# Optimization experiments

Measured on AMD Instinct MI355X. Metric: run time of the kernel, lower is better.

Reference implementation:

```python
import jax, jax.numpy as jnp
import numpy as np

MEX_C = 2.0 / (np.sqrt(3.0) * np.pi ** 0.25)

def mexican_hat(z):
    return MEX_C * (z * z - 1.0) * jnp.exp(-0.5 * z * z)

def setup_inputs() -> dict:
    key = jax.random.key(0)
    ks = jax.random.split(key, 5)
    B, T, D, O = 4, 2048, 128, 128
    x = jax.random.normal(ks[0], (B, T, D), dtype=jnp.float32)
    # init like torch: scale ~ U(0.5,1.5), translation ~ U(-0.5,0.5), kaiming-ish weights
    scale = jax.random.uniform(ks[1], (O, D), dtype=jnp.float32, minval=0.5, maxval=1.5)
    translation = jax.random.uniform(ks[2], (O, D), dtype=jnp.float32, minval=-0.5, maxval=0.5)
    bound = 1.0 / np.sqrt(D)
    wavelet_weights = jax.random.uniform(ks[3], (O, D), dtype=jnp.float32, minval=-bound, maxval=bound)
    base_w = jax.random.uniform(ks[4], (O, D), dtype=jnp.float32, minval=-bound, maxval=bound)
    ln_gamma = jnp.ones((D,), dtype=jnp.float32)
    ln_beta = jnp.zeros((D,), dtype=jnp.float32)
    return {"x": x, "scale": scale, "translation": translation,
            "wavelet_weights": wavelet_weights, "base_w": base_w,
            "ln_gamma": ln_gamma, "ln_beta": ln_beta}

def reference(x, scale, translation, wavelet_weights, base_w, ln_gamma, ln_beta):
    B, T, D = x.shape
    O = wavelet_weights.shape[0]
    # LayerNorm over last dim (eps = 1e-5, torch default)
    mu = jnp.mean(x, axis=-1, keepdims=True)
    var = jnp.mean((x - mu) ** 2, axis=-1, keepdims=True)
    x_norm = (x - mu) / jnp.sqrt(var + 1e-5) * ln_gamma + ln_beta
    x_flat = x_norm.reshape(B * T, D)                      # (N, D)
    s = jax.nn.softplus(scale) + 0.1                       # (O, D)
    # broadcast intermediate (N, O, D) — the memory-bound path
    z = (x_flat[:, None, :] - translation[None]) / s[None]
    w = jnp.clip(mexican_hat(z), -10.0, 10.0)              # (N, O, D)
    wavelet_out = jnp.einsum('nod,od->no', w, wavelet_weights)
    base_out = x.reshape(B * T, D) @ base_w.T              # base uses raw x
    out = wavelet_out + jax.nn.silu(base_out)
    return out.reshape(B, T, O)
```

## Files before the change

kernel.cpp:

```cpp
#include <hip/hip_runtime.h>


#define D_DIM 128
#define O_DIM 128
#define ROWS  16
#define BLOCK 1024
#define XSTRIDE 9

#define C1     0.72134752f
#define SQRT_C 0.84932180f
#define WWK    1.2023651f
#define LOG2E  1.44269504f

typedef float v2f __attribute__((ext_vector_type(2)));

__device__ __forceinline__ unsigned bf16r(float f) {
    unsigned u = __float_as_uint(f);
    return (u + 0x7fffu + ((u >> 16) & 1u)) >> 16;
}


__device__ __forceinline__ v2f pk_fma_xhi_nlo(v2f x, v2f w) {
    v2f d;
    asm("v_pk_fma_f32 %0, %1, %2, %2 op_sel:[0,1,0] op_sel_hi:[1,1,0] neg_lo:[0,0,1] neg_hi:[0,0,1]"
        : "=v"(d) : "v"(x), "v"(w));
    return d;
}
__device__ __forceinline__ v2f pk_mul(v2f a, v2f b) {
    v2f d;
    asm("v_pk_mul_f32 %0, %1, %2" : "=v"(d) : "v"(a), "v"(b));
    return d;
}
__device__ __forceinline__ v2f pk_sub(v2f a, v2f b) {
    v2f d;
    asm("v_pk_add_f32 %0, %1, %2 neg_lo:[0,1] neg_hi:[0,1]" : "=v"(d) : "v"(a), "v"(b));
    return d;
}
__device__ __forceinline__ void pk_fma_acc_lo(v2f& acc, v2f s, v2f w) {
    asm("v_pk_fma_f32 %0, %1, %2, %0 op_sel:[0,0,0] op_sel_hi:[1,0,1]"
        : "+v"(acc) : "v"(s), "v"(w));
}
__device__ __forceinline__ void pk_fma_acc_hi(v2f& acc, v2f s, v2f w) {
    asm("v_pk_fma_f32 %0, %1, %2, %0 op_sel:[0,1,0] op_sel_hi:[1,1,1]"
        : "+v"(acc) : "v"(s), "v"(w));
}

__global__ __launch_bounds__(256) void wavekan_prep(
    const float* __restrict__ scale,
    const float* __restrict__ trans,
    const float* __restrict__ ww,
    const float* __restrict__ bw,
    uint2* __restrict__ wsW)
{
    int idx = blockIdx.x * blockDim.x + threadIdx.x;
    if (idx >= O_DIM * D_DIM) return;
    int o = idx >> 7;
    int d = idx & (D_DIM - 1);
    float sc = scale[idx];
    float sp = fmaxf(sc, 0.0f) + log1pf(__expf(-fabsf(sc)));
    float is2 = SQRT_C / (sp + 0.1f);
    uint2 w;
    w.x = bf16r(trans[idx] * is2) | (bf16r(is2) << 16);
    w.y = bf16r(ww[idx] * WWK)    | (bf16r(bw[idx]) << 16);
    wsW[d * O_DIM + o] = w;
}

template<bool USE_WS>
__global__ __launch_bounds__(BLOCK, 8) void wavekan_main(
    const float* __restrict__ x,
    const float* __restrict__ scale,
    const float* __restrict__ trans,
    const float* __restrict__ ww,
    const float* __restrict__ bw,
    const float* __restrict__ gamma,
    const float* __restrict__ beta,
    const uint2* __restrict__ wsW,
    float* __restrict__ out,
    int N)
{
    __shared__ float4 s_x[D_DIM * XSTRIDE];

    const int tid  = threadIdx.x;
    const int row0 = blockIdx.x * ROWS;

    {
        const int r  = tid >> 6;
        const int j  = tid & 63;
        const int d0 = j * 2;
        const int grow = row0 + r;

        float2 v2 = make_float2(0.f, 0.f);
        if (grow < N)
            v2 = *reinterpret_cast<const float2*>(x + (size_t)grow * D_DIM + d0);

        float sum = v2.x + v2.y;
        float ssq = v2.x * v2.x + v2.y * v2.y;
        #pragma unroll
        for (int m = 1; m < 64; m <<= 1) {
            sum += __shfl_xor(sum, m, 64);
            ssq += __shfl_xor(ssq, m, 64);
        }
        const float mean = sum * (1.0f / D_DIM);
        const float var  = ssq * (1.0f / D_DIM) - mean * mean;
        const float rstd = rsqrtf(var + 1e-5f);

        float2 g2 = *reinterpret_cast<const float2*>(gamma + d0);
        float2 b2 = *reinterpret_cast<const float2*>(beta + d0);

        const int p  = r >> 1;
        const int h  = r & 1;
        float* c0 = reinterpret_cast<float*>(&s_x[d0 * XSTRIDE + p]);
        float* c1 = reinterpret_cast<float*>(&s_x[(d0 + 1) * XSTRIDE + p]);
        c0[h]     = (v2.x - mean) * rstd * g2.x + b2.x;
        c0[2 + h] = v2.x;
        c1[h]     = (v2.y - mean) * rstd * g2.y + b2.y;
        c1[2 + h] = v2.y;
    }
    __syncthreads();

    const int o = tid & (O_DIM - 1);
    const int g = tid >> 7;

    v2f accw = {0.f, 0.f};
    v2f accb = {0.f, 0.f};
    const v2f vC1 = {C1, C1};

    if (USE_WS) {
        uint2 w = wsW[o];
        #pragma unroll 4
        for (int d = 0; d < D_DIM; ++d) {
            uint2 wn  = wsW[(((d + 1) & (D_DIM - 1)) << 7) + o];
            float4 xx = s_x[d * XSTRIDE + g];
            v2f w01, w23;
            w01.x = __uint_as_float(w.x << 16);
            w01.y = __uint_as_float(w.x & 0xffff0000u);
            w23.x = __uint_as_float(w.y << 16);
            w23.y = __uint_as_float(w.y & 0xffff0000u);
            v2f xln = {xx.x, xx.y};
            v2f xrw = {xx.z, xx.w};

            v2f u = pk_fma_xhi_nlo(xln, w01);
            v2f q = pk_mul(u, u);
            v2f t = pk_sub(q, vC1);
            v2f e = {__builtin_amdgcn_exp2f(-q.x),
                     __builtin_amdgcn_exp2f(-q.y)};
            v2f s = pk_mul(t, e);
            pk_fma_acc_lo(accw, s, w23);
            pk_fma_acc_hi(accb, xrw, w23);
            w = wn;
        }
    } else {
        for (int d = 0; d < D_DIM; ++d) {
            int idx = o * D_DIM + d;
            float sc = scale[idx];
            float sp = fmaxf(sc, 0.0f) + log1pf(__expf(-fabsf(sc)));
            float is  = SQRT_C / (sp + 0.1f);
            float tws = trans[idx] * is;
            float wwk = ww[idx] * WWK;
            float bwv = bw[idx];
            float4 xx = s_x[d * XSTRIDE + g];
            float u0 = fmaf(xx.x, is, -tws);
            float u1 = fmaf(xx.y, is, -tws);
            float q0 = u0 * u0, q1 = u1 * u1;
            accw.x = fmaf((q0 - C1) * __builtin_amdgcn_exp2f(-q0), wwk, accw.x);
            accw.y = fmaf((q1 - C1) * __builtin_amdgcn_exp2f(-q1), wwk, accw.y);
            accb.x = fmaf(xx.z, bwv, accb.x);
            accb.y = fmaf(xx.w, bwv, accb.y);
        }
    }

    {
        const int rr0 = row0 + g * 2;
        if (rr0 < N) {
            float sig0 = 1.0f / (1.0f + __builtin_amdgcn_exp2f(-LOG2E * accb.x));
            out[(size_t)rr0 * O_DIM + o] = accw.x + accb.x * sig0;
        }
        if (rr0 + 1 < N) {
            float sig1 = 1.0f / (1.0f + __builtin_amdgcn_exp2f(-LOG2E * accb.y));
            out[(size_t)(rr0 + 1) * O_DIM + o] = accw.y + accb.y * sig1;
        }
    }
}

extern "C" void kernel_launch(void* const* d_in, const int* in_sizes, int n_in,
                              void* d_out, int out_size, void* d_ws, size_t ws_size,
                              hipStream_t stream) {
    const float* x     = (const float*)d_in[0];
    const float* scale = (const float*)d_in[1];
    const float* trans = (const float*)d_in[2];
    const float* ww    = (const float*)d_in[3];
    const float* bw    = (const float*)d_in[4];
    const float* gamma = (const float*)d_in[5];
    const float* beta  = (const float*)d_in[6];
    float* out = (float*)d_out;

    const int N = in_sizes[0] / D_DIM;
    const int grid = (N + ROWS - 1) / ROWS;

    const size_t ws_needed = (size_t)O_DIM * D_DIM * sizeof(uint2);
    if (ws_size >= ws_needed) {
        wavekan_prep<<<(O_DIM * D_DIM + 255) / 256, 256, 0, stream>>>(
            scale, trans, ww, bw, (uint2*)d_ws);
        wavekan_main<true><<<grid, BLOCK, 0, stream>>>(
            x, scale, trans, ww, bw, gamma, beta, (const uint2*)d_ws, out, N);
    } else {
        wavekan_main<false><<<grid, BLOCK, 0, stream>>>(
            x, scale, trans, ww, bw, gamma, beta, nullptr, out, N);
    }
}
```

Baseline: 101.3 us.

## Stage bf16 weights in LDS, derive base matmul from normalized x, split outputs

The main kernel now splits the output dimension into two halves per block and stages the bf16 weight table half in shared memory instead of loading it from global memory every iteration. The normalized input is stored as packed bf16, four rows per thread, and the base linear term is recovered from the normalized values by algebra (weights divided by gamma plus per-output correction sums from a new prep kernel). This lets one LDS stream feed both terms and drops the raw-x copy. The C1 subtraction is folded into an FMA. The cost is bf16 rounding of the normalized activations, a division by gamma that breaks if gamma is zero, and an extra small prep kernel launch.

After: 101.9 us. No clear change (+0.6%).

```diff
diff --git a/kernel.cpp b/kernel.cpp
--- a/kernel.cpp
+++ b/kernel.cpp
@@ -3,9 +3,9 @@
 
 #define D_DIM 128
 #define O_DIM 128
-#define ROWS  16
-#define BLOCK 1024
-#define XSTRIDE 9
+#define ROWS  32
+#define BLOCK 512
+#define OH    64
 
 #define C1     0.72134752f
 #define SQRT_C 0.84932180f
@@ -18,7 +18,6 @@
     unsigned u = __float_as_uint(f);
     return (u + 0x7fffu + ((u >> 16) & 1u)) >> 16;
 }
-
 
 __device__ __forceinline__ v2f pk_fma_xhi_nlo(v2f x, v2f w) {
     v2f d;
@@ -31,14 +30,14 @@
     asm("v_pk_mul_f32 %0, %1, %2" : "=v"(d) : "v"(a), "v"(b));
     return d;
 }
-__device__ __forceinline__ v2f pk_sub(v2f a, v2f b) {
+__device__ __forceinline__ v2f pk_fma_lolo(v2f q, v2f w, v2f c) {
     v2f d;
-    asm("v_pk_add_f32 %0, %1, %2 neg_lo:[0,1] neg_hi:[0,1]" : "=v"(d) : "v"(a), "v"(b));
+    asm("v_pk_fma_f32 %0, %1, %2, %3 op_sel:[0,0,0] op_sel_hi:[1,0,0]"
+        : "=v"(d) : "v"(q), "v"(w), "v"(c));
     return d;
 }
-__device__ __forceinline__ void pk_fma_acc_lo(v2f& acc, v2f s, v2f w) {
-    asm("v_pk_fma_f32 %0, %1, %2, %0 op_sel:[0,0,0] op_sel_hi:[1,0,1]"
-        : "+v"(acc) : "v"(s), "v"(w));
+__device__ __forceinline__ void pk_fma_vv(v2f& acc, v2f a, v2f b) {
+    asm("v_pk_fma_f32 %0, %1, %2, %0" : "+v"(acc) : "v"(a), "v"(b));
 }
 __device__ __forceinline__ void pk_fma_acc_hi(v2f& acc, v2f s, v2f w) {
     asm("v_pk_fma_f32 %0, %1, %2, %0 op_sel:[0,1,0] op_sel_hi:[1,1,1]"
@@ -50,6 +49,7 @@
     const float* __restrict__ trans,
     const float* __restrict__ ww,
     const float* __restrict__ bw,
+    const float* __restrict__ gamma,
     uint2* __restrict__ wsW)
 {
     int idx = blockIdx.x * blockDim.x + threadIdx.x;
@@ -59,14 +59,161 @@
     float sc = scale[idx];
     float sp = fmaxf(sc, 0.0f) + log1pf(__expf(-fabsf(sc)));
     float is2 = SQRT_C / (sp + 0.1f);
+    float bwg = bw[idx] / gamma[d];
     uint2 w;
     w.x = bf16r(trans[idx] * is2) | (bf16r(is2) << 16);
-    w.y = bf16r(ww[idx] * WWK)    | (bf16r(bw[idx]) << 16);
+    w.y = bf16r(ww[idx] * WWK)    | (bf16r(bwg) << 16);
     wsW[d * O_DIM + o] = w;
 }
 
-template<bool USE_WS>
-__global__ __launch_bounds__(BLOCK, 8) void wavekan_main(
+__global__ __launch_bounds__(128) void wavekan_prep2(
+    const float* __restrict__ bw,
+    const float* __restrict__ gamma,
+    const float* __restrict__ beta,
+    float2* __restrict__ cbsb)
+{
+    int o = blockIdx.x, t = threadIdx.x;
+    float b  = bw[o * D_DIM + t];
+    float bg = b / gamma[t];
+    float cb = beta[t] * bg;
+    float sb = b;
+    #pragma unroll
+    for (int m = 1; m < 64; m <<= 1) {
+        cb += __shfl_xor(cb, m, 64);
+        sb += __shfl_xor(sb, m, 64);
+    }
+    __shared__ float2 tmp[2];
+    if ((t & 63) == 0) tmp[t >> 6] = make_float2(cb, sb);
+    __syncthreads();
+    if (t == 0) cbsb[o] = make_float2(tmp[0].x + tmp[1].x, tmp[0].y + tmp[1].y);
+}
+
+__global__ __launch_bounds__(BLOCK, 4) void wavekan_main(
+    const float* __restrict__ x,
+    const uint2* __restrict__ wsW,
+    const float2* __restrict__ cbsb,
+    const float* __restrict__ gamma,
+    const float* __restrict__ beta,
+    float* __restrict__ out,
+    int N)
+{
+    __shared__ uint4  s_w4[D_DIM * OH / 2];
+    __shared__ uint2  s_ln2[8 * D_DIM];
+    __shared__ float2 s_mr[ROWS];
+
+    const int tid  = threadIdx.x;
+    const int h    = blockIdx.x & 1;
+    const int row0 = (blockIdx.x >> 1) * ROWS;
+
+    const uint4* wsW4 = reinterpret_cast<const uint4*>(wsW);
+    #pragma unroll
+    for (int k = 0; k < 8; ++k) {
+        int flat = tid + k * BLOCK;
+        int d = flat >> 5, z = flat & 31;
+        s_w4[flat] = wsW4[d * 64 + h * 32 + z];
+    }
+
+    {
+        const int r  = tid >> 4;
+        const int j  = tid & 15;
+        const int d0 = j * 8;
+        const int grow = row0 + r;
+
+        float v[8];
+        if (grow < N) {
+            const float4* p = reinterpret_cast<const float4*>(x + (size_t)grow * D_DIM + d0);
+            float4 a = p[0], b4 = p[1];
+            v[0]=a.x; v[1]=a.y; v[2]=a.z; v[3]=a.w;
+            v[4]=b4.x; v[5]=b4.y; v[6]=b4.z; v[7]=b4.w;
+        } else {
+            #pragma unroll
+            for (int k = 0; k < 8; ++k) v[k] = 0.0f;
+        }
+        float sum = 0.f, ssq = 0.f;
+        #pragma unroll
+        for (int k = 0; k < 8; ++k) { sum += v[k]; ssq += v[k] * v[k]; }
+        #pragma unroll
+        for (int m = 1; m < 16; m <<= 1) {
+            sum += __shfl_xor(sum, m, 64);
+            ssq += __shfl_xor(ssq, m, 64);
+        }
+        const float mean = sum * (1.0f / D_DIM);
+        const float var  = ssq * (1.0f / D_DIM) - mean * mean;
+        const float rstd = rsqrtf(var + 1e-5f);
+        const float sv   = (var + 1e-5f) * rstd;
+
+        const float4* pg = reinterpret_cast<const float4*>(gamma + d0);
+        const float4* pb = reinterpret_cast<const float4*>(beta + d0);
+        float4 g0 = pg[0], g1 = pg[1], b0 = pb[0], b1 = pb[1];
+        float gg[8] = {g0.x,g0.y,g0.z,g0.w,g1.x,g1.y,g1.z,g1.w};
+        float bb[8] = {b0.x,b0.y,b0.z,b0.w,b1.x,b1.y,b1.z,b1.w};
+
+        const int gi  = r >> 2;
+        const int sub = r & 3;
+        unsigned short* sl = reinterpret_cast<unsigned short*>(s_ln2);
+        #pragma unroll
+        for (int k = 0; k < 8; ++k) {
+            float ln = (v[k] - mean) * rstd * gg[k] + bb[k];
+            sl[(gi * D_DIM + d0 + k) * 4 + sub] = (unsigned short)bf16r(ln);
+        }
+        if (j == 0) s_mr[r] = make_float2(mean, sv);
+    }
+    __syncthreads();
+
+    const int lane = tid & 63;
+    const int g    = tid >> 6;
+    const int o    = h * OH + lane;
+    const uint2* __restrict__ sw = reinterpret_cast<const uint2*>(s_w4);
+
+    v2f accw01 = {0.f,0.f}, accw23 = {0.f,0.f};
+    v2f accb01 = {0.f,0.f}, accb23 = {0.f,0.f};
+    const v2f vNegC1 = {-C1, -C1};
+
+    #pragma unroll 4
+    for (int d = 0; d < D_DIM; ++d) {
+        uint2 wv = sw[d * OH + lane];
+        uint2 xv = s_ln2[g * D_DIM + d];
+        v2f w01, w23, xln01, xln23;
+        w01.x   = __uint_as_float(wv.x << 16);
+        w01.y   = __uint_as_float(wv.x & 0xffff0000u);
+        w23.x   = __uint_as_float(wv.y << 16);
+        w23.y   = __uint_as_float(wv.y & 0xffff0000u);
+        xln01.x = __uint_as_float(xv.x << 16);
+        xln01.y = __uint_as_float(xv.x & 0xffff0000u);
+        xln23.x = __uint_as_float(xv.y << 16);
+        xln23.y = __uint_as_float(xv.y & 0xffff0000u);
+
+        v2f wc  = pk_mul(w23, vNegC1);
+        v2f u01 = pk_fma_xhi_nlo(xln01, w01);
+        v2f u23 = pk_fma_xhi_nlo(xln23, w01);
+        v2f q01 = pk_mul(u01, u01);
+        v2f q23 = pk_mul(u23, u23);
+        v2f e01 = {__builtin_amdgcn_exp2f(-q01.x), __builtin_amdgcn_exp2f(-q01.y)};
+        v2f e23 = {__builtin_amdgcn_exp2f(-q23.x), __builtin_amdgcn_exp2f(-q23.y)};
+        v2f p01 = pk_fma_lolo(q01, w23, wc);
+        v2f p23 = pk_fma_lolo(q23, w23, wc);
+        pk_fma_vv(accw01, p01, e01);
+        pk_fma_vv(accw23, p23, e23);
+        pk_fma_acc_hi(accb01, xln01, w23);
+        pk_fma_acc_hi(accb23, xln23, w23);
+    }
+
+    float2 cs = cbsb[o];
+    float aw[4] = {accw01.x, accw01.y, accw23.x, accw23.y};
+    float ab[4] = {accb01.x, accb01.y, accb23.x, accb23.y};
+    #pragma unroll
+    for (int k = 0; k < 4; ++k) {
+        const int rr = row0 + g * 4 + k;
+        if (rr < N) {
+            float2 mr  = s_mr[g * 4 + k];
+            float base = (ab[k] - cs.x) * mr.y + mr.x * cs.y;
+            float sig  = 1.0f / (1.0f + __builtin_amdgcn_exp2f(-LOG2E * base));
+            out[(size_t)rr * O_DIM + o] = aw[k] + base * sig;
+        }
+    }
+}
+
+__global__ __launch_bounds__(1024, 8) void wavekan_main_fb(
     const float* __restrict__ x,
     const float* __restrict__ scale,
     const float* __restrict__ trans,
@@ -74,111 +221,55 @@
     const float* __restrict__ bw,
     const float* __restrict__ gamma,
     const float* __restrict__ beta,
-    const uint2* __restrict__ wsW,
     float* __restrict__ out,
     int N)
 {
-    __shared__ float4 s_x[D_DIM * XSTRIDE];
-
-    const int tid  = threadIdx.x;
-    const int row0 = blockIdx.x * ROWS;
-
+    __shared__ float4 s_x[128 * 9];
+    const int tid = threadIdx.x;
+    const int row0 = blockIdx.x * 16;
     {
-        const int r  = tid >> 6;
-        const int j  = tid & 63;
-        const int d0 = j * 2;
+        const int r = tid >> 6, j = tid & 63, d0 = j * 2;
         const int grow = row0 + r;
-
         float2 v2 = make_float2(0.f, 0.f);
-        if (grow < N)
-            v2 = *reinterpret_cast<const float2*>(x + (size_t)grow * D_DIM + d0);
-
-        float sum = v2.x + v2.y;
-        float ssq = v2.x * v2.x + v2.y * v2.y;
+        if (grow < N) v2 = *reinterpret_cast<const float2*>(x + (size_t)grow * D_DIM + d0);
+        float sum = v2.x + v2.y, ssq = v2.x * v2.x + v2.y * v2.y;
         #pragma unroll
-        for (int m = 1; m < 64; m <<= 1) {
-            sum += __shfl_xor(sum, m, 64);
-            ssq += __shfl_xor(ssq, m, 64);
-        }
-        const float mean = sum * (1.0f / D_DIM);
-        const float var  = ssq * (1.0f / D_DIM) - mean * mean;
+        for (int m = 1; m < 64; m <<= 1) { sum += __shfl_xor(sum, m, 64); ssq += __shfl_xor(ssq, m, 64); }
+        const float mean = sum / 128.f, var = ssq / 128.f - mean * mean;
         const float rstd = rsqrtf(var + 1e-5f);
-
         float2 g2 = *reinterpret_cast<const float2*>(gamma + d0);
         float2 b2 = *reinterpret_cast<const float2*>(beta + d0);
-
-        const int p  = r >> 1;
-        const int h  = r & 1;
-        float* c0 = reinterpret_cast<float*>(&s_x[d0 * XSTRIDE + p]);
-        float* c1 = reinterpret_cast<float*>(&s_x[(d0 + 1) * XSTRIDE + p]);
-        c0[h]     = (v2.x - mean) * rstd * g2.x + b2.x;
-        c0[2 + h] = v2.x;
-        c1[h]     = (v2.y - mean) * rstd * g2.y + b2.y;
-        c1[2 + h] = v2.y;
+        const int p = r >> 1, hh = r & 1;
+        float* c0 = reinterpret_cast<float*>(&s_x[d0 * 9 + p]);
+        float* c1 = reinterpret_cast<float*>(&s_x[(d0 + 1) * 9 + p]);
+        c0[hh] = (v2.x - mean) * rstd * g2.x + b2.x; c0[2 + hh] = v2.x;
+        c1[hh] = (v2.y - mean) * rstd * g2.y + b2.y; c1[2 + hh] = v2.y;
     }
     __syncthreads();
-
-    const int o = tid & (O_DIM - 1);
-    const int g = tid >> 7;
-
-    v2f accw = {0.f, 0.f};
-    v2f accb = {0.f, 0.f};
-    const v2f vC1 = {C1, C1};
-
-    if (USE_WS) {
-        uint2 w = wsW[o];
-        #pragma unroll 4
-        for (int d = 0; d < D_DIM; ++d) {
-            uint2 wn  = wsW[(((d + 1) & (D_DIM - 1)) << 7) + o];
-            float4 xx = s_x[d * XSTRIDE + g];
-            v2f w01, w23;
-            w01.x = __uint_as_float(w.x << 16);
-            w01.y = __uint_as_float(w.x & 0xffff0000u);
-            w23.x = __uint_as_float(w.y << 16);
-            w23.y = __uint_as_float(w.y & 0xffff0000u);
-            v2f xln = {xx.x, xx.y};
-            v2f xrw = {xx.z, xx.w};
-
-            v2f u = pk_fma_xhi_nlo(xln, w01);
-            v2f q = pk_mul(u, u);
-            v2f t = pk_sub(q, vC1);
-            v2f e = {__builtin_amdgcn_exp2f(-q.x),
-                     __builtin_amdgcn_exp2f(-q.y)};
-            v2f s = pk_mul(t, e);
-            pk_fma_acc_lo(accw, s, w23);
-            pk_fma_acc_hi(accb, xrw, w23);
-            w = wn;
-        }
-    } else {
-        for (int d = 0; d < D_DIM; ++d) {
-            int idx = o * D_DIM + d;
-            float sc = scale[idx];
-            float sp = fmaxf(sc, 0.0f) + log1pf(__expf(-fabsf(sc)));
-            float is  = SQRT_C / (sp + 0.1f);
-            float tws = trans[idx] * is;
-            float wwk = ww[idx] * WWK;
-            float bwv = bw[idx];
-            float4 xx = s_x[d * XSTRIDE + g];
-            float u0 = fmaf(xx.x, is, -tws);
-            float u1 = fmaf(xx.y, is, -tws);
-            float q0 = u0 * u0, q1 = u1 * u1;
-            accw.x = fmaf((q0 - C1) * __builtin_amdgcn_exp2f(-q0), wwk, accw.x);
-            accw.y = fmaf((q1 - C1) * __builtin_amdgcn_exp2f(-q1), wwk, accw.y);
-            accb.x = fmaf(xx.z, bwv, accb.x);
-            accb.y = fmaf(xx.w, bwv, accb.y);
-        }
-    }
-
-    {
-        const int rr0 = row0 + g * 2;
-        if (rr0 < N) {
-            float sig0 = 1.0f / (1.0f + __builtin_amdgcn_exp2f(-LOG2E * accb.x));
-            out[(size_t)rr0 * O_DIM + o] = accw.x + accb.x * sig0;
-        }
-        if (rr0 + 1 < N) {
-            float sig1 = 1.0f / (1.0f + __builtin_amdgcn_exp2f(-LOG2E * accb.y));
-            out[(size_t)(rr0 + 1) * O_DIM + o] = accw.y + accb.y * sig1;
-        }
+    const int o = tid & 127, g = tid >> 7;
+    float aw0 = 0.f, aw1 = 0.f, ab0 = 0.f, ab1 = 0.f;
+    for (int d = 0; d < D_DIM; ++d) {
+        int idx = o * D_DIM + d;
+        float sc = scale[idx];
+        float sp = fmaxf(sc, 0.0f) + log1pf(__expf(-fabsf(sc)));
+        float is = SQRT_C / (sp + 0.1f);
+        float tws = trans[idx] * is, wwk = ww[idx] * WWK, bwv = bw[idx];
+        float4 xx = s_x[d * 9 + g];
+        float u0 = fmaf(xx.x, is, -tws), u1 = fmaf(xx.y, is, -tws);
+        float q0 = u0 * u0, q1 = u1 * u1;
+        aw0 = fmaf((q0 - C1) * __builtin_amdgcn_exp2f(-q0), wwk, aw0);
+        aw1 = fmaf((q1 - C1) * __builtin_amdgcn_exp2f(-q1), wwk, aw1);
+        ab0 = fmaf(xx.z, bwv, ab0);
+        ab1 = fmaf(xx.w, bwv, ab1);
+    }
+    const int rr0 = row0 + g * 2;
+    if (rr0 < N) {
+        float s0 = 1.0f / (1.0f + __builtin_amdgcn_exp2f(-LOG2E * ab0));
+        out[(size_t)rr0 * O_DIM + o] = aw0 + ab0 * s0;
+    }
+    if (rr0 + 1 < N) {
+        float s1 = 1.0f / (1.0f + __builtin_amdgcn_exp2f(-LOG2E * ab1));
+        out[(size_t)(rr0 + 1) * O_DIM + o] = aw1 + ab1 * s1;
     }
 }
 
@@ -195,16 +286,20 @@
     float* out = (float*)d_out;
 
     const int N = in_sizes[0] / D_DIM;
-    const int grid = (N + ROWS - 1) / ROWS;
-
-    const size_t ws_needed = (size_t)O_DIM * D_DIM * sizeof(uint2);
+
+    const size_t tbl_bytes = (size_t)O_DIM * D_DIM * sizeof(uint2);
+    const size_t ws_needed = tbl_bytes + O_DIM * sizeof(float2);
     if (ws_size >= ws_needed) {
+        uint2*  tbl  = (uint2*)d_ws;
+        float2* cbsb = (float2*)((char*)d_ws + tbl_bytes);
         wavekan_prep<<<(O_DIM * D_DIM + 255) / 256, 256, 0, stream>>>(
-            scale, trans, ww, bw, (uint2*)d_ws);
-        wavekan_main<true><<<grid, BLOCK, 0, stream>>>(
-            x, scale, trans, ww, bw, gamma, beta, (const uint2*)d_ws, out, N);
+            scale, trans, ww, bw, gamma, tbl);
+        wavekan_prep2<<<O_DIM, 128, 0, stream>>>(bw, gamma, beta, cbsb);
+        const int grid = ((N + ROWS - 1) / ROWS) * 2;
+        wavekan_main<<<grid, BLOCK, 0, stream>>>(
+            x, tbl, cbsb, gamma, beta, out, N);
     } else {
-        wavekan_main<false><<<grid, BLOCK, 0, stream>>>(
-            x, scale, trans, ww, bw, gamma, beta, nullptr, out, N);
-    }
-}
+        wavekan_main_fb<<<(N + 15) / 16, 1024, 0, stream>>>(
+            x, scale, trans, ww, bw, gamma, beta, out, N);
+    }
+}
```
